# Kernel optimization log

Hardware: AMD Instinct MI355X
Metric: run time of the kernel (lower is better)

The kernel has to match this reference:

```python
import jax, jax.numpy as jnp
import numpy as np

DIM = 768
HEADS = 12
HEAD_DIM = DIM // HEADS
SCALE = HEAD_DIM ** -0.5
NEG = -65504.0


def setup_inputs() -> dict:
    key = jax.random.key(0)
    ks = jax.random.split(key, 7)
    B, N, C = 8, 1024, DIM
    x = jax.random.normal(ks[0], (B, N, C), dtype=jnp.float32)
    rel_pos_bias = jax.random.normal(ks[1], (HEADS, N, N), dtype=jnp.float32)
    attn_mask = jax.random.randint(ks[2], (B, N, N), 0, 2) == 1
    # parameters (torch nn.Linear: y = x @ W.T + b)
    W_qkv = jax.random.normal(ks[3], (3 * C, C), dtype=jnp.float32) * (C ** -0.5)
    b_qkv = jnp.zeros((3 * C,), dtype=jnp.float32)
    W_proj = jax.random.normal(ks[4], (C, C), dtype=jnp.float32) * (C ** -0.5)
    b_proj = jnp.zeros((C,), dtype=jnp.float32)
    return {"x": x, "rel_pos_bias": rel_pos_bias, "attn_mask": attn_mask,
            "W_qkv": W_qkv, "b_qkv": b_qkv, "W_proj": W_proj, "b_proj": b_proj}


def reference(x, rel_pos_bias, attn_mask, W_qkv, b_qkv, W_proj, b_proj):
    B, N, C = x.shape
    qkv = x @ W_qkv.T + b_qkv                                  # [B,N,3C]
    qkv = qkv.reshape(B, N, 3, HEADS, HEAD_DIM).transpose(2, 0, 3, 1, 4)
    q, k, v = qkv[0], qkv[1], qkv[2]                           # [B,H,N,D]
    attn = jnp.einsum('bhnd,bhmd->bhnm', q * SCALE, k)         # [B,H,N,N]
    attn = jnp.where(attn_mask[:, None, :, :], NEG, attn)
    attn = attn + rel_pos_bias[None]                           # bias broadcast over B
    attn_wo_softmax = attn
    p = jax.nn.softmax(attn, axis=-1)                          # attn_drop p=0 (eval)
    out = jnp.einsum('bhnm,bhmd->bhnd', p, v)
    out = out.transpose(0, 2, 1, 3).reshape(B, N, C)
    out = out @ W_proj.T + b_proj                              # proj_drop p=0
    return out, attn_wo_softmax
```

## Files before the change

kernel.cpp:

```cpp
#include <hip/hip_runtime.h>
#include <hip/hip_bf16.h>

typedef __attribute__((ext_vector_type(8))) short bf16x8;
typedef __attribute__((ext_vector_type(4))) short bf16x4;
typedef __attribute__((ext_vector_type(4))) float f32x4;

#define MFMA32(a,b,c) __builtin_amdgcn_mfma_f32_16x16x32_bf16(a,b,c,0,0,0)

#if __has_builtin(__builtin_amdgcn_mfma_f32_16x16x16bf16_1k)
#define MFMA16(a,b,c) __builtin_amdgcn_mfma_f32_16x16x16bf16_1k(a,b,c,0,0,0)
#else
static __device__ __forceinline__ f32x4 mfma16_asm(bf16x4 a, bf16x4 b, f32x4 c){
  asm volatile("v_mfma_f32_16x16x16_bf16 %0, %1, %2, %0" : "+v"(c) : "v"(a), "v"(b));
  return c;
}
#define MFMA16(a,b,c) mfma16_asm(a,b,c)
#endif

#define NEGV -65504.0f

__device__ __forceinline__ unsigned short f2bf(float f){
  union { float f; unsigned u; } x; x.f = f;
  unsigned r = x.u + 0x7fffu + ((x.u >> 16) & 1u);
  return (unsigned short)(r >> 16);
}

__device__ __forceinline__ unsigned cvtpk(float a, float b){
  unsigned r;
  asm volatile("v_cvt_pk_bf16_f32 %0, %1, %2" : "=v"(r) : "v"(a), "v"(b));
  return r;
}

__global__ void cvt_all(const float* __restrict__ x, const float* __restrict__ wq,
                        const float* __restrict__ wp, unsigned short* __restrict__ out){
  int i = blockIdx.x * 256 + threadIdx.x;
  const float* src; int j;
  if (i < 1572864)      { src = x;  j = i; }
  else if (i < 2015232) { src = wq; j = i - 1572864; }
  else                  { src = wp; j = i - 2015232; }
  float4 f = ((const float4*)src)[j];
  ushort4 u;
  u.x = f2bf(f.x); u.y = f2bf(f.y); u.z = f2bf(f.z); u.w = f2bf(f.w);
  ((ushort4*)out)[i] = u;
}

__global__ __launch_bounds__(256) void mask_to_bits(const int* __restrict__ m,
                                                    unsigned long long* __restrict__ out){
  int gw = (blockIdx.x * 256 + threadIdx.x) >> 6;
  int lane = threadIdx.x & 63;
#pragma unroll
  for (int stp = 0; stp < 16; ++stp) {
    size_t base = ((size_t)gw * 16 + stp) * 64;
    int v = m[base + lane];
    unsigned long long bb = __ballot(v != 0);
    if (lane == 0) out[base >> 6] = bb;
  }
}

__global__ __launch_bounds__(256) void gemm_qkv(
    const unsigned short* __restrict__ X,
    const unsigned short* __restrict__ W,
    const float* __restrict__ bias,
    unsigned short* __restrict__ Qd,
    unsigned short* __restrict__ Kd,
    unsigned short* __restrict__ Vd)
{
  __shared__ unsigned short As[128*40];
  __shared__ unsigned short Bs[128*40];
  const int K = 768;
  int tid = threadIdx.x;
  int bm = blockIdx.x & 63;
  int bn = blockIdx.x >> 6;
  int wave = tid >> 6, lane = tid & 63;
  int lo = lane & 15, g = lane >> 4;
  int wr = (wave >> 1) * 64, wc = (wave & 1) * 64;
  int row0 = bm * 128, col0 = bn * 128;

  int sr = tid >> 1;
  int sc = (tid & 1) * 16;
  const unsigned short* gA = X + (size_t)(row0 + sr) * K + sc;
  const unsigned short* gB = W + (size_t)(col0 + sr) * K + sc;
  unsigned short* sA = &As[sr * 40 + sc];
  unsigned short* sB = &Bs[sr * 40 + sc];

  f32x4 acc[4][4] = {};
  for (int k0 = 0; k0 < K; k0 += 32) {
    bf16x8 a0 = *(const bf16x8*)(gA + k0);
    bf16x8 a1 = *(const bf16x8*)(gA + k0 + 8);
    bf16x8 b0 = *(const bf16x8*)(gB + k0);
    bf16x8 b1 = *(const bf16x8*)(gB + k0 + 8);
    __syncthreads();
    *(bf16x8*)(sA)     = a0;
    *(bf16x8*)(sA + 8) = a1;
    *(bf16x8*)(sB)     = b0;
    *(bf16x8*)(sB + 8) = b1;
    __syncthreads();
    bf16x8 af[4], bf[4];
#pragma unroll
    for (int i = 0; i < 4; ++i) af[i] = *(const bf16x8*)&As[(wr + i*16 + lo)*40 + g*8];
#pragma unroll
    for (int i = 0; i < 4; ++i) bf[i] = *(const bf16x8*)&Bs[(wc + i*16 + lo)*40 + g*8];
#pragma unroll
    for (int mi = 0; mi < 4; ++mi)
#pragma unroll
      for (int ni = 0; ni < 4; ++ni)
        acc[mi][ni] = MFMA32(af[mi], bf[ni], acc[mi][ni]);
  }
  int orow0 = row0 + wr, ocol0 = col0 + wc;
#pragma unroll
  for (int ni = 0; ni < 4; ++ni) {
    int col = ocol0 + ni*16 + lo;
    float bc = bias[col];
    int which = col / 768;
    int rem = col - which * 768;
    int h = rem >> 6, d = rem & 63;
    unsigned short* dst = (which == 0) ? Qd : (which == 1) ? Kd : Vd;
    float scale = (which == 0) ? 0.125f : 1.0f;
#pragma unroll
    for (int mi = 0; mi < 4; ++mi) {
#pragma unroll
      for (int r = 0; r < 4; ++r) {
        int row = orow0 + mi*16 + g*4 + r;
        int bb = row >> 10, n = row & 1023;
        dst[(((size_t)bb*12 + h)*1024 + n)*64 + d] = f2bf((acc[mi][ni][r] + bc) * scale);
      }
    }
  }
}

__global__ __launch_bounds__(256) void vtrans(const unsigned short* __restrict__ V,
                                              unsigned short* __restrict__ Vt){
  __shared__ unsigned short t[64][72];
  int bh = blockIdx.y;
  int n0 = blockIdx.x * 64;
  int tid = threadIdx.x;
  int nl = tid >> 2;
  int dq = (tid & 3) * 16;
  const unsigned short* src = V + ((size_t)bh*1024 + n0 + nl)*64 + dq;
  bf16x8 a0 = *(const bf16x8*)(src);
  bf16x8 a1 = *(const bf16x8*)(src + 8);
  *(bf16x8*)&t[nl][dq]     = a0;
  *(bf16x8*)&t[nl][dq + 8] = a1;
  __syncthreads();
  int d  = tid >> 2;
  int nq = (tid & 3) * 16;
  union { unsigned short s[16]; bf16x8 v[2]; } pk;
#pragma unroll
  for (int j = 0; j < 16; ++j) pk.s[j] = t[nq + j][d];
  unsigned short* dst = Vt + ((size_t)bh*64 + d)*1024 + n0 + nq;
  *(bf16x8*)(dst)     = pk.v[0];
  *(bf16x8*)(dst + 8) = pk.v[1];
}

__global__ __launch_bounds__(512, 4) void attn_kernel(
    const unsigned short* __restrict__ Qd,
    const unsigned short* __restrict__ Kd,
    const unsigned short* __restrict__ Vt,
    const float* __restrict__ bias,
    const unsigned* __restrict__ maskbits,
    float* __restrict__ out1,
    unsigned short* __restrict__ ctx)
{
  __shared__ char lds[32768];
  const int N = 1024, D = 64;
  int y = blockIdx.y;
  int h = y >> 3, bb = y & 7;
  int bh = bb * 12 + h;
  int tid = threadIdx.x;
  int wave = tid >> 6, lane = tid & 63;
  int lo = lane & 15, g = lane >> 4;
  int qrow = blockIdx.x * 128 + wave * 16 + lo;

  const size_t qoff = ((size_t)bh * N + qrow) * D;
  bf16x8 qf0 = *(const bf16x8*)(Qd + qoff + g*8);
  bf16x8 qf1 = *(const bf16x8*)(Qd + qoff + 32 + g*8);

  const float* bias_row = bias + ((size_t)h * N + qrow) * N;
  const unsigned* mrow  = maskbits + ((size_t)bb * N + qrow) * 32;
  float* out_row        = out1 + ((size_t)bh * N + qrow) * N;

  int o  = tid * 16;
  int sw = o ^ (((o >> 7) & 7) << 4);
  const char* kbase = (const char*)(Kd + (size_t)bh * N * D);
  const char* vbase = (const char*)(Vt + (size_t)bh * D * N);
  const char* ksrc  = kbase + sw;
  const char* vsrc  = vbase + (o >> 7) * 2048 + (sw & 127);
  int wbase = (tid >> 6) << 10;

#define STAGE(buf, kv) do { \
    __builtin_amdgcn_global_load_lds( \
      (const __attribute__((address_space(1))) unsigned*)(ksrc + (size_t)(kv)*128), \
      (__attribute__((address_space(3))) unsigned*)(lds + (buf)*8192 + wbase), 16, 0, 0); \
    __builtin_amdgcn_global_load_lds( \
      (const __attribute__((address_space(1))) unsigned*)(vsrc + (size_t)(kv)*2), \
      (__attribute__((address_space(3))) unsigned*)(lds + 16384 + (buf)*8192 + wbase), 16, 0, 0); \
  } while (0)

#define SWZ(lb) ((lb) ^ ((((lb) >> 7) & 7) << 4))

  float m_run = -INFINITY, l_part = 0.0f;
  f32x4 oacc[4] = {};

  STAGE(0, 0);
  __syncthreads();
  int cur = 0;

  for (int it = 0; it < 16; ++it) {
    int kv = it * 64;
    if (it < 15) STAGE(cur ^ 1, kv + 64);
    __builtin_amdgcn_sched_barrier(0);

    unsigned mw0 = mrow[it*2];
    unsigned mw1 = mrow[it*2 + 1];

    f32x4 s[4];
    __builtin_amdgcn_s_setprio(1);
#pragma unroll
    for (int sub = 0; sub < 4; ++sub) {
      int lbr = (sub*16 + lo) * 128 + g*16;
      bf16x8 k0 = *(const bf16x8*)(lds + cur*8192 + SWZ(lbr));
      bf16x8 k1 = *(const bf16x8*)(lds + cur*8192 + SWZ(lbr + 64));
      f32x4 t = {};
      t = MFMA32(k0, qf0, t);
      t = MFMA32(k1, qf1, t);
      s[sub] = t;
    }
    __builtin_amdgcn_s_setprio(0);

    float sp[16];
#pragma unroll
    for (int sub = 0; sub < 4; ++sub) {
      f32x4 bi = *(const f32x4*)(bias_row + kv + sub*16 + g*4);
      unsigned mw = (sub < 2) ? mw0 : mw1;
      int sh = (sub & 1) * 16 + g * 4;
#pragma unroll
      for (int r = 0; r < 4; ++r)
        sp[sub*4+r] = (((mw >> (sh + r)) & 1u) ? NEGV : s[sub][r]) + bi[r];
      f32x4 ov;
      ov[0] = sp[sub*4]; ov[1] = sp[sub*4+1]; ov[2] = sp[sub*4+2]; ov[3] = sp[sub*4+3];
      __builtin_nontemporal_store(ov, (f32x4*)(out_row + kv + sub*16 + g*4));
    }

    float lmax = sp[0];
#pragma unroll
    for (int i = 1; i < 16; ++i) lmax = fmaxf(lmax, sp[i]);
    if (!__all(lmax <= m_run + 8.0f)) {
      float tmax = fmaxf(lmax, __shfl_xor(lmax, 16));
      tmax = fmaxf(tmax, __shfl_xor(tmax, 32));
      float mnew = fmaxf(m_run, tmax);
      float alpha = __expf(m_run - mnew);
      l_part *= alpha;
#pragma unroll
      for (int c = 0; c < 4; ++c) {
        oacc[c][0] *= alpha; oacc[c][1] *= alpha;
        oacc[c][2] *= alpha; oacc[c][3] *= alpha;
      }
      m_run = mnew;
    }
    float lsum = 0.0f;
#pragma unroll
    for (int i = 0; i < 16; ++i) { sp[i] = __expf(sp[i] - m_run); lsum += sp[i]; }
    l_part += lsum;

    union { unsigned u[2]; bf16x4 h; } pk[4];
#pragma unroll
    for (int ks = 0; ks < 4; ++ks) {
      pk[ks].u[0] = cvtpk(sp[ks*4],   sp[ks*4+1]);
      pk[ks].u[1] = cvtpk(sp[ks*4+2], sp[ks*4+3]);
    }

    __builtin_amdgcn_s_setprio(1);
#pragma unroll
    for (int ks = 0; ks < 4; ++ks)
#pragma unroll
      for (int c = 0; c < 4; ++c) {
        int lbv = (c*16 + lo) * 128 + ks*32 + g*8;
        bf16x4 vf = *(const bf16x4*)(lds + 16384 + cur*8192 + SWZ(lbv));
        oacc[c] = MFMA16(vf, pk[ks].h, oacc[c]);
      }
    __builtin_amdgcn_s_setprio(0);

    cur ^= 1;
    __builtin_amdgcn_sched_barrier(0);
    asm volatile("s_waitcnt vmcnt(4)" ::: "memory");
    __builtin_amdgcn_s_barrier();
  }

  l_part += __shfl_xor(l_part, 16);
  l_part += __shfl_xor(l_part, 32);
  float inv = 1.0f / l_part;

  size_t crow = ((size_t)bb * N + qrow) * 768 + h * 64;
#pragma unroll
  for (int c = 0; c < 4; ++c) {
    ushort4 u;
    u.x = f2bf(oacc[c][0] * inv);
    u.y = f2bf(oacc[c][1] * inv);
    u.z = f2bf(oacc[c][2] * inv);
    u.w = f2bf(oacc[c][3] * inv);
    *(ushort4*)(ctx + crow + c*16 + g*4) = u;
  }
#undef STAGE
#undef SWZ
}

__global__ __launch_bounds__(256) void gemm_proj(
    const unsigned short* __restrict__ X,
    const unsigned short* __restrict__ W,
    const float* __restrict__ bias,
    float* __restrict__ out)
{
  __shared__ unsigned short As[128*40];
  __shared__ unsigned short Bs[128*40];
  const int K = 768;
  int tid = threadIdx.x;
  int bm = blockIdx.x & 63;
  int bn = blockIdx.x >> 6;
  int wave = tid >> 6, lane = tid & 63;
  int lo = lane & 15, g = lane >> 4;
  int wr = (wave >> 1) * 64, wc = (wave & 1) * 64;
  int row0 = bm * 128, col0 = bn * 128;

  int sr = tid >> 1;
  int sc = (tid & 1) * 16;
  const unsigned short* gA = X + (size_t)(row0 + sr) * K + sc;
  const unsigned short* gB = W + (size_t)(col0 + sr) * K + sc;
  unsigned short* sA = &As[sr * 40 + sc];
  unsigned short* sB = &Bs[sr * 40 + sc];

  f32x4 acc[4][4] = {};
  for (int k0 = 0; k0 < K; k0 += 32) {
    bf16x8 a0 = *(const bf16x8*)(gA + k0);
    bf16x8 a1 = *(const bf16x8*)(gA + k0 + 8);
    bf16x8 b0 = *(const bf16x8*)(gB + k0);
    bf16x8 b1 = *(const bf16x8*)(gB + k0 + 8);
    __syncthreads();
    *(bf16x8*)(sA)     = a0;
    *(bf16x8*)(sA + 8) = a1;
    *(bf16x8*)(sB)     = b0;
    *(bf16x8*)(sB + 8) = b1;
    __syncthreads();
    bf16x8 af[4], bf[4];
#pragma unroll
    for (int i = 0; i < 4; ++i) af[i] = *(const bf16x8*)&As[(wr + i*16 + lo)*40 + g*8];
#pragma unroll
    for (int i = 0; i < 4; ++i) bf[i] = *(const bf16x8*)&Bs[(wc + i*16 + lo)*40 + g*8];
#pragma unroll
    for (int mi = 0; mi < 4; ++mi)
#pragma unroll
      for (int ni = 0; ni < 4; ++ni)
        acc[mi][ni] = MFMA32(af[mi], bf[ni], acc[mi][ni]);
  }
  int orow0 = row0 + wr, ocol0 = col0 + wc;
#pragma unroll
  for (int ni = 0; ni < 4; ++ni) {
    int col = ocol0 + ni*16 + lo;
    float bc = bias[col];
#pragma unroll
    for (int mi = 0; mi < 4; ++mi) {
#pragma unroll
      for (int r = 0; r < 4; ++r) {
        int row = orow0 + mi*16 + g*4 + r;
        out[(size_t)row * 768 + col] = acc[mi][ni][r] + bc;
      }
    }
  }
}

extern "C" void kernel_launch(void* const* d_in, const int* in_sizes, int n_in,
                              void* d_out, int out_size, void* d_ws, size_t ws_size,
                              hipStream_t stream) {
  const float* x            = (const float*)d_in[0];
  const float* rel_pos_bias = (const float*)d_in[1];
  const int* mask           = (const int*)d_in[2];
  const float* Wqkv         = (const float*)d_in[3];
  const float* bqkv         = (const float*)d_in[4];
  const float* Wproj        = (const float*)d_in[5];
  const float* bproj        = (const float*)d_in[6];

  float* out0 = (float*)d_out;
  float* out1 = out0 + (size_t)8 * 1024 * 768;

  char* ws = (char*)d_ws;
  unsigned short* xb  = (unsigned short*)(ws);
  unsigned short* wqb = (unsigned short*)(ws + 12582912);
  unsigned short* wpb = (unsigned short*)(ws + 16121856);
  unsigned short* Qb  = (unsigned short*)(ws + 17301504);
  unsigned short* Kb  = (unsigned short*)(ws + 29884416);
  unsigned short* Vb  = (unsigned short*)(ws + 42467328);
  unsigned short* ctx = (unsigned short*)(ws + 55050240);
  unsigned short* Vtb = xb;
  unsigned long long* mbits = (unsigned long long*)(ws + 12582912);

  cvt_all<<<8448, 256, 0, stream>>>(x, Wqkv, Wproj, xb);

  gemm_qkv<<<1152, 256, 0, stream>>>(xb, wqb, bqkv, Qb, Kb, Vb);

  mask_to_bits<<<2048, 256, 0, stream>>>(mask, mbits);

  vtrans<<<dim3(16, 96), 256, 0, stream>>>(Vb, Vtb);

  attn_kernel<<<dim3(8, 96), 512, 0, stream>>>(Qb, Kb, Vtb, rel_pos_bias,
                                               (const unsigned*)mbits, out1, ctx);

  gemm_proj<<<384, 256, 0, stream>>>(ctx, wpb, bproj, out0);
}
```

Baseline: 233.7 us.

## Process two query tiles per wave to reuse K/V LDS fragments

The attention kernel drops from 8 to 4 waves per block, and each wave now handles 32 query rows as two 16-row tiles. Each K and V fragment read from LDS then feeds two MFMAs, halving LDS reads per unit of compute, while each thread issues twice as many global-to-LDS copies. Bias and mask loads are also hoisted to the top of each iteration, ahead of the K/V prefetch, so their latency can overlap the MFMA work. The cost is higher register pressure, with two accumulator sets and two score arrays, and fewer waves per block to hide latency.

```diff
diff --git a/kernel.cpp b/kernel.cpp
--- a/kernel.cpp
+++ b/kernel.cpp
@@ -152,7 +152,7 @@
   *(bf16x8*)(dst + 8) = pk.v[1];
 }
 
-__global__ __launch_bounds__(512, 4) void attn_kernel(
+__global__ __launch_bounds__(256, 3) void attn_kernel(
     const unsigned short* __restrict__ Qd,
     const unsigned short* __restrict__ Kd,
     const unsigned short* __restrict__ Vt,
@@ -169,15 +169,22 @@
   int tid = threadIdx.x;
   int wave = tid >> 6, lane = tid & 63;
   int lo = lane & 15, g = lane >> 4;
-  int qrow = blockIdx.x * 128 + wave * 16 + lo;
-
-  const size_t qoff = ((size_t)bh * N + qrow) * D;
-  bf16x8 qf0 = *(const bf16x8*)(Qd + qoff + g*8);
-  bf16x8 qf1 = *(const bf16x8*)(Qd + qoff + 32 + g*8);
-
-  const float* bias_row = bias + ((size_t)h * N + qrow) * N;
-  const unsigned* mrow  = maskbits + ((size_t)bb * N + qrow) * 32;
-  float* out_row        = out1 + ((size_t)bh * N + qrow) * N;
+  int q0 = blockIdx.x * 128 + wave * 32;
+  int qrow0 = q0 + lo, qrow1 = q0 + 16 + lo;
+
+  const size_t qo0 = ((size_t)bh * N + qrow0) * D;
+  const size_t qo1 = ((size_t)bh * N + qrow1) * D;
+  bf16x8 qf00 = *(const bf16x8*)(Qd + qo0 + g*8);
+  bf16x8 qf01 = *(const bf16x8*)(Qd + qo0 + 32 + g*8);
+  bf16x8 qf10 = *(const bf16x8*)(Qd + qo1 + g*8);
+  bf16x8 qf11 = *(const bf16x8*)(Qd + qo1 + 32 + g*8);
+
+  const float* br0 = bias + ((size_t)h * N + qrow0) * N;
+  const float* br1 = bias + ((size_t)h * N + qrow1) * N;
+  const unsigned* mr0 = maskbits + ((size_t)bb * N + qrow0) * 32;
+  const unsigned* mr1 = maskbits + ((size_t)bb * N + qrow1) * 32;
+  float* or0 = out1 + ((size_t)bh * N + qrow0) * N;
+  float* or1 = out1 + ((size_t)bh * N + qrow1) * N;
 
   int o  = tid * 16;
   int sw = o ^ (((o >> 7) & 7) << 4);
@@ -185,21 +192,22 @@
   const char* vbase = (const char*)(Vt + (size_t)bh * D * N);
   const char* ksrc  = kbase + sw;
   const char* vsrc  = vbase + (o >> 7) * 2048 + (sw & 127);
-  int wbase = (tid >> 6) << 10;
-
+  int wbase = wave << 10;
+
+#define GLL(src, dst) __builtin_amdgcn_global_load_lds( \
+      (const __attribute__((address_space(1))) unsigned*)(src), \
+      (__attribute__((address_space(3))) unsigned*)(dst), 16, 0, 0)
 #define STAGE(buf, kv) do { \
-    __builtin_amdgcn_global_load_lds( \
-      (const __attribute__((address_space(1))) unsigned*)(ksrc + (size_t)(kv)*128), \
-      (__attribute__((address_space(3))) unsigned*)(lds + (buf)*8192 + wbase), 16, 0, 0); \
-    __builtin_amdgcn_global_load_lds( \
-      (const __attribute__((address_space(1))) unsigned*)(vsrc + (size_t)(kv)*2), \
-      (__attribute__((address_space(3))) unsigned*)(lds + 16384 + (buf)*8192 + wbase), 16, 0, 0); \
+    GLL(ksrc + (size_t)(kv)*128,          lds + (buf)*8192 + wbase); \
+    GLL(ksrc + (size_t)(kv)*128 + 4096,   lds + (buf)*8192 + wbase + 4096); \
+    GLL(vsrc + (size_t)(kv)*2,            lds + 16384 + (buf)*8192 + wbase); \
+    GLL(vsrc + (size_t)(kv)*2 + 65536,    lds + 16384 + (buf)*8192 + wbase + 4096); \
   } while (0)
 
 #define SWZ(lb) ((lb) ^ ((((lb) >> 7) & 7) << 4))
 
-  float m_run = -INFINITY, l_part = 0.0f;
-  f32x4 oacc[4] = {};
+  float m0 = -INFINITY, m1 = -INFINITY, l0 = 0.0f, l1 = 0.0f;
+  f32x4 oacc0[4] = {}, oacc1[4] = {};
 
   STAGE(0, 0);
   __syncthreads();
@@ -207,66 +215,81 @@
 
   for (int it = 0; it < 16; ++it) {
     int kv = it * 64;
+
+    uint2 mwa = *(const uint2*)(mr0 + it*2);
+    uint2 mwb = *(const uint2*)(mr1 + it*2);
+    f32x4 bi0[4], bi1[4];
+#pragma unroll
+    for (int sub = 0; sub < 4; ++sub) {
+      bi0[sub] = *(const f32x4*)(br0 + kv + sub*16 + g*4);
+      bi1[sub] = *(const f32x4*)(br1 + kv + sub*16 + g*4);
+    }
+    __builtin_amdgcn_sched_barrier(0);
     if (it < 15) STAGE(cur ^ 1, kv + 64);
     __builtin_amdgcn_sched_barrier(0);
 
-    unsigned mw0 = mrow[it*2];
-    unsigned mw1 = mrow[it*2 + 1];
-
-    f32x4 s[4];
+    f32x4 s0[4], s1[4];
     __builtin_amdgcn_s_setprio(1);
 #pragma unroll
     for (int sub = 0; sub < 4; ++sub) {
       int lbr = (sub*16 + lo) * 128 + g*16;
       bf16x8 k0 = *(const bf16x8*)(lds + cur*8192 + SWZ(lbr));
       bf16x8 k1 = *(const bf16x8*)(lds + cur*8192 + SWZ(lbr + 64));
-      f32x4 t = {};
-      t = MFMA32(k0, qf0, t);
-      t = MFMA32(k1, qf1, t);
-      s[sub] = t;
+      f32x4 t = {}; t = MFMA32(k0, qf00, t); t = MFMA32(k1, qf01, t); s0[sub] = t;
+      f32x4 u = {}; u = MFMA32(k0, qf10, u); u = MFMA32(k1, qf11, u); s1[sub] = u;
     }
     __builtin_amdgcn_s_setprio(0);
 
-    float sp[16];
+    float sp0[16], sp1[16];
 #pragma unroll
     for (int sub = 0; sub < 4; ++sub) {
-      f32x4 bi = *(const f32x4*)(bias_row + kv + sub*16 + g*4);
-      unsigned mw = (sub < 2) ? mw0 : mw1;
+      unsigned mw0s = (sub < 2) ? mwa.x : mwa.y;
+      unsigned mw1s = (sub < 2) ? mwb.x : mwb.y;
       int sh = (sub & 1) * 16 + g * 4;
 #pragma unroll
-      for (int r = 0; r < 4; ++r)
-        sp[sub*4+r] = (((mw >> (sh + r)) & 1u) ? NEGV : s[sub][r]) + bi[r];
-      f32x4 ov;
-      ov[0] = sp[sub*4]; ov[1] = sp[sub*4+1]; ov[2] = sp[sub*4+2]; ov[3] = sp[sub*4+3];
-      __builtin_nontemporal_store(ov, (f32x4*)(out_row + kv + sub*16 + g*4));
-    }
-
-    float lmax = sp[0];
-#pragma unroll
-    for (int i = 1; i < 16; ++i) lmax = fmaxf(lmax, sp[i]);
-    if (!__all(lmax <= m_run + 8.0f)) {
-      float tmax = fmaxf(lmax, __shfl_xor(lmax, 16));
-      tmax = fmaxf(tmax, __shfl_xor(tmax, 32));
-      float mnew = fmaxf(m_run, tmax);
-      float alpha = __expf(m_run - mnew);
-      l_part *= alpha;
+      for (int r = 0; r < 4; ++r) {
+        sp0[sub*4+r] = (((mw0s >> (sh + r)) & 1u) ? NEGV : s0[sub][r]) + bi0[sub][r];
+        sp1[sub*4+r] = (((mw1s >> (sh + r)) & 1u) ? NEGV : s1[sub][r]) + bi1[sub][r];
+      }
+      f32x4 ov0, ov1;
+      ov0[0]=sp0[sub*4]; ov0[1]=sp0[sub*4+1]; ov0[2]=sp0[sub*4+2]; ov0[3]=sp0[sub*4+3];
+      ov1[0]=sp1[sub*4]; ov1[1]=sp1[sub*4+1]; ov1[2]=sp1[sub*4+2]; ov1[3]=sp1[sub*4+3];
+      __builtin_nontemporal_store(ov0, (f32x4*)(or0 + kv + sub*16 + g*4));
+      __builtin_nontemporal_store(ov1, (f32x4*)(or1 + kv + sub*16 + g*4));
+    }
+
+    float lx0 = sp0[0], lx1 = sp1[0];
+#pragma unroll
+    for (int i = 1; i < 16; ++i) { lx0 = fmaxf(lx0, sp0[i]); lx1 = fmaxf(lx1, sp1[i]); }
+    bool ok = (lx0 <= m0 + 8.0f) && (lx1 <= m1 + 8.0f);
+    if (!__all(ok)) {
+      float t0 = fmaxf(lx0, __shfl_xor(lx0, 16)); t0 = fmaxf(t0, __shfl_xor(t0, 32));
+      float t1 = fmaxf(lx1, __shfl_xor(lx1, 16)); t1 = fmaxf(t1, __shfl_xor(t1, 32));
+      float n0 = fmaxf(m0, t0), n1 = fmaxf(m1, t1);
+      float a0 = __expf(m0 - n0), a1 = __expf(m1 - n1);
+      l0 *= a0; l1 *= a1;
 #pragma unroll
       for (int c = 0; c < 4; ++c) {
-        oacc[c][0] *= alpha; oacc[c][1] *= alpha;
-        oacc[c][2] *= alpha; oacc[c][3] *= alpha;
+        oacc0[c][0]*=a0; oacc0[c][1]*=a0; oacc0[c][2]*=a0; oacc0[c][3]*=a0;
+        oacc1[c][0]*=a1; oacc1[c][1]*=a1; oacc1[c][2]*=a1; oacc1[c][3]*=a1;
       }
-      m_run = mnew;
-    }
-    float lsum = 0.0f;
-#pragma unroll
-    for (int i = 0; i < 16; ++i) { sp[i] = __expf(sp[i] - m_run); lsum += sp[i]; }
-    l_part += lsum;
-
-    union { unsigned u[2]; bf16x4 h; } pk[4];
+      m0 = n0; m1 = n1;
+    }
+    float ls0 = 0.0f, ls1 = 0.0f;
+#pragma unroll
+    for (int i = 0; i < 16; ++i) {
+      sp0[i] = __expf(sp0[i] - m0); ls0 += sp0[i];
+      sp1[i] = __expf(sp1[i] - m1); ls1 += sp1[i];
+    }
+    l0 += ls0; l1 += ls1;
+
+    union { unsigned u[2]; bf16x4 h; } pk0[4], pk1[4];
 #pragma unroll
     for (int ks = 0; ks < 4; ++ks) {
-      pk[ks].u[0] = cvtpk(sp[ks*4],   sp[ks*4+1]);
-      pk[ks].u[1] = cvtpk(sp[ks*4+2], sp[ks*4+3]);
+      pk0[ks].u[0] = cvtpk(sp0[ks*4],   sp0[ks*4+1]);
+      pk0[ks].u[1] = cvtpk(sp0[ks*4+2], sp0[ks*4+3]);
+      pk1[ks].u[0] = cvtpk(sp1[ks*4],   sp1[ks*4+1]);
+      pk1[ks].u[1] = cvtpk(sp1[ks*4+2], sp1[ks*4+3]);
     }
 
     __builtin_amdgcn_s_setprio(1);
@@ -276,31 +299,35 @@
       for (int c = 0; c < 4; ++c) {
         int lbv = (c*16 + lo) * 128 + ks*32 + g*8;
         bf16x4 vf = *(const bf16x4*)(lds + 16384 + cur*8192 + SWZ(lbv));
-        oacc[c] = MFMA16(vf, pk[ks].h, oacc[c]);
+        oacc0[c] = MFMA16(vf, pk0[ks].h, oacc0[c]);
+        oacc1[c] = MFMA16(vf, pk1[ks].h, oacc1[c]);
       }
     __builtin_amdgcn_s_setprio(0);
 
     cur ^= 1;
     __builtin_amdgcn_sched_barrier(0);
-    asm volatile("s_waitcnt vmcnt(4)" ::: "memory");
+    asm volatile("s_waitcnt vmcnt(8)" ::: "memory");
     __builtin_amdgcn_s_barrier();
   }
 
-  l_part += __shfl_xor(l_part, 16);
-  l_part += __shfl_xor(l_part, 32);
-  float inv = 1.0f / l_part;
-
-  size_t crow = ((size_t)bb * N + qrow) * 768 + h * 64;
+  l0 += __shfl_xor(l0, 16); l0 += __shfl_xor(l0, 32);
+  l1 += __shfl_xor(l1, 16); l1 += __shfl_xor(l1, 32);
+  float inv0 = 1.0f / l0, inv1 = 1.0f / l1;
+
+  size_t crow0 = ((size_t)bb * N + qrow0) * 768 + h * 64;
+  size_t crow1 = ((size_t)bb * N + qrow1) * 768 + h * 64;
 #pragma unroll
   for (int c = 0; c < 4; ++c) {
-    ushort4 u;
-    u.x = f2bf(oacc[c][0] * inv);
-    u.y = f2bf(oacc[c][1] * inv);
-    u.z = f2bf(oacc[c][2] * inv);
-    u.w = f2bf(oacc[c][3] * inv);
-    *(ushort4*)(ctx + crow + c*16 + g*4) = u;
+    ushort4 u0, u1;
+    u0.x = f2bf(oacc0[c][0] * inv0); u0.y = f2bf(oacc0[c][1] * inv0);
+    u0.z = f2bf(oacc0[c][2] * inv0); u0.w = f2bf(oacc0[c][3] * inv0);
+    u1.x = f2bf(oacc1[c][0] * inv1); u1.y = f2bf(oacc1[c][1] * inv1);
+    u1.z = f2bf(oacc1[c][2] * inv1); u1.w = f2bf(oacc1[c][3] * inv1);
+    *(ushort4*)(ctx + crow0 + c*16 + g*4) = u0;
+    *(ushort4*)(ctx + crow1 + c*16 + g*4) = u1;
   }
 #undef STAGE
+#undef GLL
 #undef SWZ
 }
 
@@ -400,7 +427,7 @@
 
   vtrans<<<dim3(16, 96), 256, 0, stream>>>(Vb, Vtb);
 
-  attn_kernel<<<dim3(8, 96), 512, 0, stream>>>(Qb, Kb, Vtb, rel_pos_bias,
+  attn_kernel<<<dim3(8, 96), 256, 0, stream>>>(Qb, Kb, Vtb, rel_pos_bias,
                                                (const unsigned*)mbits, out1, ctx);
 
   gemm_proj<<<384, 256, 0, stream>>>(ctx, wpb, bproj, out0);
```

New measurement: 295.3 us. 1.26x slower.

## Fuse mask packing into convert kernel and write V transposed from QKV GEMM

Applied to the files above, without the earlier changes.

Merges the fp32-to-bf16 conversion and mask bit-packing into one launch. It also removes the separate V transpose kernel by having the QKV GEMM epilogue write V directly in transposed layout as 4-wide vector stores. In the attention loop, the mask words and bias tile loads are issued before the next K/V stage prefetch, so their latency overlaps the score MFMAs. This cuts two kernel launches and a round trip of V through memory, at the cost of strided epilogue stores for the V columns and a new workspace offset for the mask bits.

```diff
diff --git a/kernel.cpp b/kernel.cpp
--- a/kernel.cpp
+++ b/kernel.cpp
@@ -31,29 +31,31 @@
   return r;
 }
 
-__global__ void cvt_all(const float* __restrict__ x, const float* __restrict__ wq,
-                        const float* __restrict__ wp, unsigned short* __restrict__ out){
-  int i = blockIdx.x * 256 + threadIdx.x;
-  const float* src; int j;
-  if (i < 1572864)      { src = x;  j = i; }
-  else if (i < 2015232) { src = wq; j = i - 1572864; }
-  else                  { src = wp; j = i - 2015232; }
-  float4 f = ((const float4*)src)[j];
-  ushort4 u;
-  u.x = f2bf(f.x); u.y = f2bf(f.y); u.z = f2bf(f.z); u.w = f2bf(f.w);
-  ((ushort4*)out)[i] = u;
-}
-
-__global__ __launch_bounds__(256) void mask_to_bits(const int* __restrict__ m,
-                                                    unsigned long long* __restrict__ out){
-  int gw = (blockIdx.x * 256 + threadIdx.x) >> 6;
-  int lane = threadIdx.x & 63;
-#pragma unroll
-  for (int stp = 0; stp < 16; ++stp) {
-    size_t base = ((size_t)gw * 16 + stp) * 64;
-    int v = m[base + lane];
-    unsigned long long bb = __ballot(v != 0);
-    if (lane == 0) out[base >> 6] = bb;
+__global__ __launch_bounds__(256) void cvt_mask(
+    const float* __restrict__ x, const float* __restrict__ wq,
+    const float* __restrict__ wp, unsigned short* __restrict__ out,
+    const int* __restrict__ m, unsigned long long* __restrict__ mb){
+  int bid = blockIdx.x;
+  if (bid < 8448) {
+    int i = bid * 256 + threadIdx.x;
+    const float* src; int j;
+    if (i < 1572864)      { src = x;  j = i; }
+    else if (i < 2015232) { src = wq; j = i - 1572864; }
+    else                  { src = wp; j = i - 2015232; }
+    float4 f = ((const float4*)src)[j];
+    ushort4 u;
+    u.x = f2bf(f.x); u.y = f2bf(f.y); u.z = f2bf(f.z); u.w = f2bf(f.w);
+    ((ushort4*)out)[i] = u;
+  } else {
+    int gw = ((bid - 8448) * 256 + threadIdx.x) >> 6;
+    int lane = threadIdx.x & 63;
+#pragma unroll
+    for (int stp = 0; stp < 16; ++stp) {
+      size_t base = ((size_t)gw * 16 + stp) * 64;
+      int v = m[base + lane];
+      unsigned long long bbm = __ballot(v != 0);
+      if (lane == 0) mb[base >> 6] = bbm;
+    }
   }
 }
 
@@ -63,7 +65,7 @@
     const float* __restrict__ bias,
     unsigned short* __restrict__ Qd,
     unsigned short* __restrict__ Kd,
-    unsigned short* __restrict__ Vd)
+    unsigned short* __restrict__ Vtd)
 {
   __shared__ unsigned short As[128*40];
   __shared__ unsigned short Bs[128*40];
@@ -114,42 +116,32 @@
     int which = col / 768;
     int rem = col - which * 768;
     int h = rem >> 6, d = rem & 63;
-    unsigned short* dst = (which == 0) ? Qd : (which == 1) ? Kd : Vd;
-    float scale = (which == 0) ? 0.125f : 1.0f;
-#pragma unroll
-    for (int mi = 0; mi < 4; ++mi) {
-#pragma unroll
-      for (int r = 0; r < 4; ++r) {
-        int row = orow0 + mi*16 + g*4 + r;
+    if (which == 2) {
+#pragma unroll
+      for (int mi = 0; mi < 4; ++mi) {
+        int row = orow0 + mi*16 + g*4;
         int bb = row >> 10, n = row & 1023;
-        dst[(((size_t)bb*12 + h)*1024 + n)*64 + d] = f2bf((acc[mi][ni][r] + bc) * scale);
-      }
-    }
-  }
-}
-
-__global__ __launch_bounds__(256) void vtrans(const unsigned short* __restrict__ V,
-                                              unsigned short* __restrict__ Vt){
-  __shared__ unsigned short t[64][72];
-  int bh = blockIdx.y;
-  int n0 = blockIdx.x * 64;
-  int tid = threadIdx.x;
-  int nl = tid >> 2;
-  int dq = (tid & 3) * 16;
-  const unsigned short* src = V + ((size_t)bh*1024 + n0 + nl)*64 + dq;
-  bf16x8 a0 = *(const bf16x8*)(src);
-  bf16x8 a1 = *(const bf16x8*)(src + 8);
-  *(bf16x8*)&t[nl][dq]     = a0;
-  *(bf16x8*)&t[nl][dq + 8] = a1;
-  __syncthreads();
-  int d  = tid >> 2;
-  int nq = (tid & 3) * 16;
-  union { unsigned short s[16]; bf16x8 v[2]; } pk;
-#pragma unroll
-  for (int j = 0; j < 16; ++j) pk.s[j] = t[nq + j][d];
-  unsigned short* dst = Vt + ((size_t)bh*64 + d)*1024 + n0 + nq;
-  *(bf16x8*)(dst)     = pk.v[0];
-  *(bf16x8*)(dst + 8) = pk.v[1];
+        ushort4 u;
+        u.x = f2bf(acc[mi][ni][0] + bc);
+        u.y = f2bf(acc[mi][ni][1] + bc);
+        u.z = f2bf(acc[mi][ni][2] + bc);
+        u.w = f2bf(acc[mi][ni][3] + bc);
+        *(ushort4*)&Vtd[(((size_t)bb*12 + h)*64 + d)*1024 + n] = u;
+      }
+    } else {
+      unsigned short* dst = (which == 0) ? Qd : Kd;
+      float scale = (which == 0) ? 0.125f : 1.0f;
+#pragma unroll
+      for (int mi = 0; mi < 4; ++mi) {
+#pragma unroll
+        for (int r = 0; r < 4; ++r) {
+          int row = orow0 + mi*16 + g*4 + r;
+          int bb = row >> 10, n = row & 1023;
+          dst[(((size_t)bb*12 + h)*1024 + n)*64 + d] = f2bf((acc[mi][ni][r] + bc) * scale);
+        }
+      }
+    }
+  }
 }
 
 __global__ __launch_bounds__(512, 4) void attn_kernel(
@@ -185,7 +177,7 @@
   const char* vbase = (const char*)(Vt + (size_t)bh * D * N);
   const char* ksrc  = kbase + sw;
   const char* vsrc  = vbase + (o >> 7) * 2048 + (sw & 127);
-  int wbase = (tid >> 6) << 10;
+  int wbase = wave << 10;
 
 #define STAGE(buf, kv) do { \
     __builtin_amdgcn_global_load_lds( \
@@ -207,11 +199,15 @@
 
   for (int it = 0; it < 16; ++it) {
     int kv = it * 64;
-    if (it < 15) STAGE(cur ^ 1, kv + 64);
+
+    uint2 mw = *(const uint2*)(mrow + it*2);
+    f32x4 bi[4];
+#pragma unroll
+    for (int sub = 0; sub < 4; ++sub)
+      bi[sub] = *(const f32x4*)(bias_row + kv + sub*16 + g*4);
     __builtin_amdgcn_sched_barrier(0);
-
-    unsigned mw0 = mrow[it*2];
-    unsigned mw1 = mrow[it*2 + 1];
+    STAGE(cur ^ 1, kv + 64);
+    __builtin_amdgcn_sched_barrier(0);
 
     f32x4 s[4];
     __builtin_amdgcn_s_setprio(1);
@@ -230,12 +226,11 @@
     float sp[16];
 #pragma unroll
     for (int sub = 0; sub < 4; ++sub) {
-      f32x4 bi = *(const f32x4*)(bias_row + kv + sub*16 + g*4);
-      unsigned mw = (sub < 2) ? mw0 : mw1;
+      unsigned mws = (sub < 2) ? mw.x : mw.y;
       int sh = (sub & 1) * 16 + g * 4;
 #pragma unroll
       for (int r = 0; r < 4; ++r)
-        sp[sub*4+r] = (((mw >> (sh + r)) & 1u) ? NEGV : s[sub][r]) + bi[r];
+        sp[sub*4+r] = (((mws >> (sh + r)) & 1u) ? NEGV : s[sub][r]) + bi[sub][r];
       f32x4 ov;
       ov[0] = sp[sub*4]; ov[1] = sp[sub*4+1]; ov[2] = sp[sub*4+2]; ov[3] = sp[sub*4+3];
       __builtin_nontemporal_store(ov, (f32x4*)(out_row + kv + sub*16 + g*4));
@@ -262,7 +257,7 @@
     for (int i = 0; i < 16; ++i) { sp[i] = __expf(sp[i] - m_run); lsum += sp[i]; }
     l_part += lsum;
 
-    union { unsigned u[2]; bf16x4 h; } pk[4];
+    union { unsigned u[2]; bf16x4 hh; } pk[4];
 #pragma unroll
     for (int ks = 0; ks < 4; ++ks) {
       pk[ks].u[0] = cvtpk(sp[ks*4],   sp[ks*4+1]);
@@ -276,7 +271,7 @@
       for (int c = 0; c < 4; ++c) {
         int lbv = (c*16 + lo) * 128 + ks*32 + g*8;
         bf16x4 vf = *(const bf16x4*)(lds + 16384 + cur*8192 + SWZ(lbv));
-        oacc[c] = MFMA16(vf, pk[ks].h, oacc[c]);
+        oacc[c] = MFMA16(vf, pk[ks].hh, oacc[c]);
       }
     __builtin_amdgcn_s_setprio(0);
 
@@ -387,18 +382,13 @@
   unsigned short* wpb = (unsigned short*)(ws + 16121856);
   unsigned short* Qb  = (unsigned short*)(ws + 17301504);
   unsigned short* Kb  = (unsigned short*)(ws + 29884416);
-  unsigned short* Vb  = (unsigned short*)(ws + 42467328);
+  unsigned short* Vtb = (unsigned short*)(ws + 42467328);
   unsigned short* ctx = (unsigned short*)(ws + 55050240);
-  unsigned short* Vtb = xb;
-  unsigned long long* mbits = (unsigned long long*)(ws + 12582912);
-
-  cvt_all<<<8448, 256, 0, stream>>>(x, Wqkv, Wproj, xb);
-
-  gemm_qkv<<<1152, 256, 0, stream>>>(xb, wqb, bqkv, Qb, Kb, Vb);
-
-  mask_to_bits<<<2048, 256, 0, stream>>>(mask, mbits);
-
-  vtrans<<<dim3(16, 96), 256, 0, stream>>>(Vb, Vtb);
+  unsigned long long* mbits = (unsigned long long*)(ws + 67633152);
+
+  cvt_mask<<<10496, 256, 0, stream>>>(x, Wqkv, Wproj, xb, mask, mbits);
+
+  gemm_qkv<<<1152, 256, 0, stream>>>(xb, wqb, bqkv, Qb, Kb, Vtb);
 
   attn_kernel<<<dim3(8, 96), 512, 0, stream>>>(Qb, Kb, Vtb, rel_pos_bias,
                                                (const unsigned*)mbits, out1, ctx);
```

After: 247.4 us. 5.9% more time.

## Prefetch bias and mask one tile ahead in attention; fuse mask packing into convert

Applied to the files above, without the earlier changes.

Attention now loads the next KV tile's rel_pos_bias and mask bits during the current tile. The scheduling barriers and a relaxed vmcnt wait let these global loads overlap with MFMA and softmax work instead of stalling right before use. The mask bit-packing kernel is merged into the fp32-to-bf16 convert launch and its buffer moved to its own workspace region, saving a launch. The launch-bounds occupancy hint rises from 4 to 8, which tightens the register budget and risks spills, and the last iteration issues a redundant wrap-around prefetch.

```diff
diff --git a/kernel.cpp b/kernel.cpp
--- a/kernel.cpp
+++ b/kernel.cpp
@@ -31,29 +31,31 @@
   return r;
 }
 
-__global__ void cvt_all(const float* __restrict__ x, const float* __restrict__ wq,
-                        const float* __restrict__ wp, unsigned short* __restrict__ out){
-  int i = blockIdx.x * 256 + threadIdx.x;
-  const float* src; int j;
-  if (i < 1572864)      { src = x;  j = i; }
-  else if (i < 2015232) { src = wq; j = i - 1572864; }
-  else                  { src = wp; j = i - 2015232; }
-  float4 f = ((const float4*)src)[j];
-  ushort4 u;
-  u.x = f2bf(f.x); u.y = f2bf(f.y); u.z = f2bf(f.z); u.w = f2bf(f.w);
-  ((ushort4*)out)[i] = u;
-}
-
-__global__ __launch_bounds__(256) void mask_to_bits(const int* __restrict__ m,
-                                                    unsigned long long* __restrict__ out){
-  int gw = (blockIdx.x * 256 + threadIdx.x) >> 6;
-  int lane = threadIdx.x & 63;
-#pragma unroll
-  for (int stp = 0; stp < 16; ++stp) {
-    size_t base = ((size_t)gw * 16 + stp) * 64;
-    int v = m[base + lane];
-    unsigned long long bb = __ballot(v != 0);
-    if (lane == 0) out[base >> 6] = bb;
+__global__ __launch_bounds__(256) void cvt_mask(
+    const float* __restrict__ x, const float* __restrict__ wq,
+    const float* __restrict__ wp, unsigned short* __restrict__ out,
+    const int* __restrict__ m, unsigned long long* __restrict__ mb){
+  int bid = blockIdx.x;
+  if (bid < 8448) {
+    int i = bid * 256 + threadIdx.x;
+    const float* src; int j;
+    if (i < 1572864)      { src = x;  j = i; }
+    else if (i < 2015232) { src = wq; j = i - 1572864; }
+    else                  { src = wp; j = i - 2015232; }
+    float4 f = ((const float4*)src)[j];
+    ushort4 u;
+    u.x = f2bf(f.x); u.y = f2bf(f.y); u.z = f2bf(f.z); u.w = f2bf(f.w);
+    ((ushort4*)out)[i] = u;
+  } else {
+    int gw = ((bid - 8448) * 256 + threadIdx.x) >> 6;
+    int lane = threadIdx.x & 63;
+#pragma unroll
+    for (int stp = 0; stp < 16; ++stp) {
+      size_t base = ((size_t)gw * 16 + stp) * 64;
+      int v = m[base + lane];
+      unsigned long long bbm = __ballot(v != 0);
+      if (lane == 0) mb[base >> 6] = bbm;
+    }
   }
 }
 
@@ -152,7 +154,7 @@
   *(bf16x8*)(dst + 8) = pk.v[1];
 }
 
-__global__ __launch_bounds__(512, 4) void attn_kernel(
+__global__ __launch_bounds__(512, 8) void attn_kernel(
     const unsigned short* __restrict__ Qd,
     const unsigned short* __restrict__ Kd,
     const unsigned short* __restrict__ Vt,
@@ -185,7 +187,7 @@
   const char* vbase = (const char*)(Vt + (size_t)bh * D * N);
   const char* ksrc  = kbase + sw;
   const char* vsrc  = vbase + (o >> 7) * 2048 + (sw & 127);
-  int wbase = (tid >> 6) << 10;
+  int wbase = wave << 10;
 
 #define STAGE(buf, kv) do { \
     __builtin_amdgcn_global_load_lds( \
@@ -201,17 +203,21 @@
   float m_run = -INFINITY, l_part = 0.0f;
   f32x4 oacc[4] = {};
 
+  uint2 mw = *(const uint2*)(mrow);
+  f32x4 bi[4];
+#pragma unroll
+  for (int sub = 0; sub < 4; ++sub)
+    bi[sub] = *(const f32x4*)(bias_row + sub*16 + g*4);
   STAGE(0, 0);
   __syncthreads();
   int cur = 0;
 
   for (int it = 0; it < 16; ++it) {
     int kv = it * 64;
-    if (it < 15) STAGE(cur ^ 1, kv + 64);
+    int kvn = ((it + 1) & 15) << 6;
+
+    STAGE(cur ^ 1, kvn);
     __builtin_amdgcn_sched_barrier(0);
-
-    unsigned mw0 = mrow[it*2];
-    unsigned mw1 = mrow[it*2 + 1];
 
     f32x4 s[4];
     __builtin_amdgcn_s_setprio(1);
@@ -230,12 +236,22 @@
     float sp[16];
 #pragma unroll
     for (int sub = 0; sub < 4; ++sub) {
-      f32x4 bi = *(const f32x4*)(bias_row + kv + sub*16 + g*4);
-      unsigned mw = (sub < 2) ? mw0 : mw1;
+      unsigned mws = (sub < 2) ? mw.x : mw.y;
       int sh = (sub & 1) * 16 + g * 4;
 #pragma unroll
       for (int r = 0; r < 4; ++r)
-        sp[sub*4+r] = (((mw >> (sh + r)) & 1u) ? NEGV : s[sub][r]) + bi[r];
+        sp[sub*4+r] = (((mws >> (sh + r)) & 1u) ? NEGV : s[sub][r]) + bi[sub][r];
+    }
+    __builtin_amdgcn_sched_barrier(0);
+
+    mw = *(const uint2*)(mrow + (kvn >> 5));
+#pragma unroll
+    for (int sub = 0; sub < 4; ++sub)
+      bi[sub] = *(const f32x4*)(bias_row + kvn + sub*16 + g*4);
+    __builtin_amdgcn_sched_barrier(0);
+
+#pragma unroll
+    for (int sub = 0; sub < 4; ++sub) {
       f32x4 ov;
       ov[0] = sp[sub*4]; ov[1] = sp[sub*4+1]; ov[2] = sp[sub*4+2]; ov[3] = sp[sub*4+3];
       __builtin_nontemporal_store(ov, (f32x4*)(out_row + kv + sub*16 + g*4));
@@ -262,7 +278,7 @@
     for (int i = 0; i < 16; ++i) { sp[i] = __expf(sp[i] - m_run); lsum += sp[i]; }
     l_part += lsum;
 
-    union { unsigned u[2]; bf16x4 h; } pk[4];
+    union { unsigned u[2]; bf16x4 hh; } pk[4];
 #pragma unroll
     for (int ks = 0; ks < 4; ++ks) {
       pk[ks].u[0] = cvtpk(sp[ks*4],   sp[ks*4+1]);
@@ -276,13 +292,13 @@
       for (int c = 0; c < 4; ++c) {
         int lbv = (c*16 + lo) * 128 + ks*32 + g*8;
         bf16x4 vf = *(const bf16x4*)(lds + 16384 + cur*8192 + SWZ(lbv));
-        oacc[c] = MFMA16(vf, pk[ks].h, oacc[c]);
+        oacc[c] = MFMA16(vf, pk[ks].hh, oacc[c]);
       }
     __builtin_amdgcn_s_setprio(0);
 
     cur ^= 1;
     __builtin_amdgcn_sched_barrier(0);
-    asm volatile("s_waitcnt vmcnt(4)" ::: "memory");
+    asm volatile("s_waitcnt vmcnt(9)" ::: "memory");
     __builtin_amdgcn_s_barrier();
   }
 
@@ -390,13 +406,11 @@
   unsigned short* Vb  = (unsigned short*)(ws + 42467328);
   unsigned short* ctx = (unsigned short*)(ws + 55050240);
   unsigned short* Vtb = xb;
-  unsigned long long* mbits = (unsigned long long*)(ws + 12582912);
-
-  cvt_all<<<8448, 256, 0, stream>>>(x, Wqkv, Wproj, xb);
+  unsigned long long* mbits = (unsigned long long*)(ws + 67633152);
+
+  cvt_mask<<<10496, 256, 0, stream>>>(x, Wqkv, Wproj, xb, mask, mbits);
 
   gemm_qkv<<<1152, 256, 0, stream>>>(xb, wqb, bqkv, Qb, Kb, Vb);
-
-  mask_to_bits<<<2048, 256, 0, stream>>>(mask, mbits);
 
   vtrans<<<dim3(16, 96), 256, 0, stream>>>(Vb, Vtb);
 
```

After: 515.3 us. 121% more time.
